# Performance work log

Hardware: AMD Instinct MI355X
Metric: run time of the kernel (lower is better)

The kernel has to match this reference:

```python
import jax, jax.numpy as jnp
import numpy as np

N_HEAD = 16
WINDOW = 256


def setup_inputs() -> dict:
    key = jax.random.key(0)
    ks = jax.random.split(key, 3)
    B, S, D = 2, 2048, 1024
    x = jax.random.normal(ks[0], (B, S, D), dtype=jnp.float32)
    w_attn = jax.random.normal(ks[1], (D, 3 * D), dtype=jnp.float32) * 0.02
    b_attn = jnp.zeros((3 * D,), dtype=jnp.float32)
    w_proj = jax.random.normal(ks[2], (D, D), dtype=jnp.float32) * 0.02
    b_proj = jnp.zeros((D,), dtype=jnp.float32)
    return {"x": x, "w_attn": w_attn, "b_attn": b_attn, "w_proj": w_proj, "b_proj": b_proj}


def reference(x, w_attn, b_attn, w_proj, b_proj):
    B, S, D = x.shape
    hd = D // N_HEAD  # head dim
    scale = 1.0 / np.sqrt(hd).astype(np.float32)

    # fused QKV projection (Conv1D == linear on last dim)
    c = jnp.einsum('bsd,df->bsf', x, w_attn) + b_attn
    q, k, v = jnp.split(c, 3, axis=-1)

    def split_heads(t):  # [B,S,D] -> [B,H,S,hd]
        return t.reshape(B, S, N_HEAD, hd).transpose(0, 2, 1, 3)

    q, k, v = split_heads(q), split_heads(k), split_heads(v)
    present = jnp.stack([k, v], axis=1)  # [B,2,H,S,hd]

    # scores [B,H,S,S]
    w = jnp.einsum('bhqd,bhkd->bhqk', q, k) * scale

    # causal sliding-window mask
    q_pos = jnp.arange(S)[:, None]
    k_pos = jnp.arange(S)[None, :]
    mask = (k_pos <= q_pos) & (k_pos >= q_pos - WINDOW + 1)  # [S,S]
    w = jnp.where(mask[None, None], w, jnp.finfo(w.dtype).min)
    w = jax.nn.softmax(w, axis=-1)

    a = jnp.einsum('bhqk,bhkd->bhqd', w, v)
    a = a.transpose(0, 2, 1, 3).reshape(B, S, D)  # merge heads
    out = jnp.einsum('bsd,df->bsf', a, w_proj) + b_proj
    return out, present
```

## Files before the change

### kernel.cpp

```cpp
#include <hip/hip_runtime.h>
#include <cstdint>
#include <cstddef>

typedef __bf16 bf16x8 __attribute__((ext_vector_type(8)));
typedef float f32x4 __attribute__((ext_vector_type(4)));

#define MFMA16(a, b, c) __builtin_amdgcn_mfma_f32_16x16x32_bf16(a, b, c, 0, 0, 0)

static __device__ __forceinline__ bf16x8 ld_bf16x8(const __bf16* p) {
    return *reinterpret_cast<const bf16x8*>(p);
}

static __device__ __forceinline__ void async_cp16(const __bf16* g, __bf16* l) {
    __builtin_amdgcn_global_load_lds((const __attribute__((address_space(1))) void*)g,
                                     (__attribute__((address_space(3))) void*)l, 16, 0, 0);
}

template <int N>
static __device__ __forceinline__ void wait_vmcnt() {
    asm volatile("s_waitcnt vmcnt(%0)" ::"n"(N) : "memory");
}

static __device__ __forceinline__ void barrier_pinned() {
    __builtin_amdgcn_sched_barrier(0);
    __builtin_amdgcn_s_barrier();
    __builtin_amdgcn_sched_barrier(0);
}

template <int CTRL>
static __device__ __forceinline__ float dppmv(float x) {
    return __builtin_bit_cast(float, __builtin_amdgcn_update_dpp(
        0, __builtin_bit_cast(int, x), CTRL, 0xF, 0xF, true));
}
static __device__ __forceinline__ float rmax16(float x) {
    x = fmaxf(x, dppmv<0x121>(x));
    x = fmaxf(x, dppmv<0x122>(x));
    x = fmaxf(x, dppmv<0x124>(x));
    x = fmaxf(x, dppmv<0x128>(x));
    return x;
}
static __device__ __forceinline__ float rsum16(float x) {
    x += dppmv<0x121>(x);
    x += dppmv<0x122>(x);
    x += dppmv<0x124>(x);
    x += dppmv<0x128>(x);
    return x;
}

__global__ void cvt_kernel(const float* __restrict__ src, __bf16* __restrict__ dst, int n8) {
    int i = blockIdx.x * blockDim.x + threadIdx.x;
    if (i >= n8) return;
    const float4* s4 = reinterpret_cast<const float4*>(src) + (size_t)i * 2;
    float4 a = s4[0], b = s4[1];
    bf16x8 o;
    o[0] = (__bf16)a.x; o[1] = (__bf16)a.y; o[2] = (__bf16)a.z; o[3] = (__bf16)a.w;
    o[4] = (__bf16)b.x; o[5] = (__bf16)b.y; o[6] = (__bf16)b.z; o[7] = (__bf16)b.w;
    reinterpret_cast<bf16x8*>(dst)[i] = o;
}

__global__ __launch_bounds__(256) void tcvt_kernel(const float* __restrict__ in,
                                                   __bf16* __restrict__ out, int K, int N) {
    __shared__ __bf16 T[64][72];
    const int k0 = blockIdx.y * 64, n0 = blockIdx.x * 64;
    const int t = threadIdx.x;
    const int col = (t & 15) << 2;
    const int rowb = t >> 4;
    #pragma unroll
    for (int i = 0; i < 4; i++) {
        int row = i * 16 + rowb;
        float4 v = *reinterpret_cast<const float4*>(&in[(size_t)(k0 + row) * N + n0 + col]);
        T[col + 0][row] = (__bf16)v.x;
        T[col + 1][row] = (__bf16)v.y;
        T[col + 2][row] = (__bf16)v.z;
        T[col + 3][row] = (__bf16)v.w;
    }
    __syncthreads();
    const int oc = (t & 7) << 3;
    const int orb = t >> 3;
    #pragma unroll
    for (int i = 0; i < 2; i++) {
        int r = i * 32 + orb;
        bf16x8 v = *reinterpret_cast<bf16x8*>(&T[r][oc]);
        *reinterpret_cast<bf16x8*>(&out[(size_t)(n0 + r) * K + k0 + oc]) = v;
    }
}

__device__ __forceinline__ void gemm_mainloop(const __bf16* __restrict__ A,
                                              const __bf16* __restrict__ Bt,
                                              int K, int row0, int col0,
                                              __bf16* Als, __bf16* Bls, f32x4 acc[4][4]) {
    const int tid = threadIdx.x;
    const int lane = tid & 63;
    const int wid = tid >> 6;
    const int wr = wid >> 1, wc = wid & 1;
    const int r0 = tid >> 2, o0 = (tid & 3) << 3;
    const __bf16* a0 = A + (size_t)(row0 + r0) * K + o0;
    const __bf16* a1 = A + (size_t)(row0 + r0 + 64) * K + o0;
    const __bf16* b0 = Bt + (size_t)(col0 + r0) * K + o0;
    const __bf16* b1 = Bt + (size_t)(col0 + r0 + 64) * K + o0;
    const int loff = tid * 8;
    const int aoff = (wr * 64 + (lane & 15)) * 32 + ((lane >> 4) << 3);
    const int boff = (wc * 64 + (lane & 15)) * 32 + ((lane >> 4) << 3);

    const int nt = K >> 5;
    async_cp16(a0, &Als[loff]);
    async_cp16(a1, &Als[loff + 2048]);
    async_cp16(b0, &Bls[loff]);
    async_cp16(b1, &Bls[loff + 2048]);
    __syncthreads();

    int cur = 0;
    for (int t = 0; t < nt; ++t) {
        if (t + 1 < nt) {
            const int k1 = (t + 1) << 5;
            const int nb = (cur ^ 1) * 4096;
            async_cp16(a0 + k1, &Als[nb + loff]);
            async_cp16(a1 + k1, &Als[nb + loff + 2048]);
            async_cp16(b0 + k1, &Bls[nb + loff]);
            async_cp16(b1 + k1, &Bls[nb + loff + 2048]);
        }
        const int cb = cur * 4096;
        bf16x8 af[4], bfr[4];
        #pragma unroll
        for (int m = 0; m < 4; m++) af[m] = ld_bf16x8(&Als[cb + aoff + m * 512]);
        #pragma unroll
        for (int n = 0; n < 4; n++) bfr[n] = ld_bf16x8(&Bls[cb + boff + n * 512]);
        #pragma unroll
        for (int m = 0; m < 4; m++) {
            #pragma unroll
            for (int n = 0; n < 4; n++) {
                acc[m][n] = MFMA16(af[m], bfr[n], acc[m][n]);
            }
        }
        __syncthreads();
        cur ^= 1;
    }
}

__global__ __launch_bounds__(256) void gemm_qkv_kernel(const __bf16* __restrict__ xb,
                                                       const __bf16* __restrict__ wabt,
                                                       const float* __restrict__ bias,
                                                       __bf16* __restrict__ qb,
                                                       __bf16* __restrict__ kb,
                                                       __bf16* __restrict__ vt,
                                                       float* __restrict__ present) {
    __shared__ __bf16 Als[2 * 128 * 32];
    __shared__ __bf16 Bls[2 * 128 * 32];
    f32x4 acc[4][4] = {};
    const int row0 = blockIdx.y * 128, col0 = blockIdx.x * 128;
    gemm_mainloop(xb, wabt, 1024, row0, col0, Als, Bls, acc);

    const int lane = threadIdx.x & 63, wid = threadIdx.x >> 6;
    const int wr = wid >> 1, wc = wid & 1;
    const int part = col0 >> 10;
    #pragma unroll
    for (int n = 0; n < 4; n++) {
        int col = col0 + wc * 64 + n * 16 + (lane & 15);
        int hh = (col >> 6) & 15;
        int dd = col & 63;
        float bv = bias[col];
        #pragma unroll
        for (int m = 0; m < 4; m++) {
            #pragma unroll
            for (int r = 0; r < 4; r++) {
                int row = row0 + wr * 64 + m * 16 + ((lane >> 4) << 2) + r;
                int bb = row >> 11, ss = row & 2047;
                float val = acc[m][n][r] + bv;
                size_t qi = (((size_t)(bb * 16 + hh)) * 2048 + ss) * 64 + dd;
                if (part == 0) {
                    qb[qi] = (__bf16)val;
                } else if (part == 1) {
                    kb[qi] = (__bf16)val;
                    present[(((size_t)((bb * 2 + 0) * 16 + hh)) * 2048 + ss) * 64 + dd] = val;
                } else {
                    vt[(((size_t)(bb * 16 + hh)) * 64 + dd) * 2048 + ss] = (__bf16)val;
                    present[(((size_t)((bb * 2 + 1) * 16 + hh)) * 2048 + ss) * 64 + dd] = val;
                }
            }
        }
    }
}

template <int BM, int BN, int WM, int WN>
__device__ __forceinline__ void mainloop2(const __bf16* __restrict__ A,
                                          const __bf16* __restrict__ Bt,
                                          int K, int row0, int col0,
                                          __bf16* lds,
                                          f32x4 (&acc)[BM / WM / 16][BN / WN / 16]) {
    constexpr int MR = BM / WM / 16, NR = BN / WN / 16;
    constexpr int AE = BM * 32;
    constexpr int BUFE = AE + BN * 32;
    constexpr int AI = BM / 16;
    constexpr int BI = BN / 16;
    constexpr int APW = AI / 8;
    constexpr int BPW = BI / 8;
    const int tid = threadIdx.x, l = tid & 63, w = tid >> 6;
    const int wm = w / WN, wn = w % WN;
    const int lr = l >> 2, lc = (l & 3) << 3;
    const int fr = l & 15, fc = (l >> 4) << 3;

    const size_t arow = (size_t)(row0 + lr) * K + lc;
    const size_t brow = (size_t)(col0 + lr) * K + lc;
    const int nt = K >> 5;

    auto stage = [&](int t, int buf) {
        const int k0 = t << 5;
        const int bb = buf * BUFE;
        #pragma unroll
        for (int j = 0; j < APW; j++) {
            const int mi = w * APW + j;
            async_cp16(A + arow + (size_t)mi * 16 * K + k0, lds + bb + mi * 512 + l * 8);
        }
        #pragma unroll
        for (int j = 0; j < BPW; j++) {
            const int ni = w * BPW + j;
            async_cp16(Bt + brow + (size_t)ni * 16 * K + k0, lds + bb + AE + ni * 512 + l * 8);
        }
    };

    stage(0, 0);
    stage(1, 1);

    const int aoff = (wm * (BM / WM) + fr) * 32 + fc;
    const int boff = AE + (wn * (BN / WN) + fr) * 32 + fc;

    int p = 0;
    for (int t = 0; t < nt; ++t) {
        if (t + 1 < nt) {
            wait_vmcnt<APW + BPW>();
        } else {
            wait_vmcnt<0>();
        }
        barrier_pinned();
        if (t + 2 < nt) {
            int p2 = p + 2; if (p2 >= 3) p2 -= 3;
            stage(t + 2, p2);
        }
        const int cb = p * BUFE;
        bf16x8 af[MR], bfv[NR];
        #pragma unroll
        for (int m = 0; m < MR; m++) af[m] = ld_bf16x8(&lds[cb + aoff + m * 512]);
        #pragma unroll
        for (int n = 0; n < NR; n++) bfv[n] = ld_bf16x8(&lds[cb + boff + n * 512]);
        __builtin_amdgcn_s_setprio(1);
        #pragma unroll
        for (int m = 0; m < MR; m++) {
            #pragma unroll
            for (int n = 0; n < NR; n++) {
                acc[m][n] = MFMA16(af[m], bfv[n], acc[m][n]);
            }
        }
        __builtin_amdgcn_s_setprio(0);
        asm volatile("s_waitcnt lgkmcnt(0)" ::: "memory");
        __builtin_amdgcn_sched_barrier(0);
        p = (p == 2) ? 0 : p + 1;
    }
}

__global__ __launch_bounds__(512, 2) void gemm_proj_kernel(const __bf16* __restrict__ ab,
                                                           const __bf16* __restrict__ wpbt,
                                                           const float* __restrict__ bias,
                                                           float* __restrict__ out) {
    __shared__ __bf16 lds[3 * (128 * 32 + 128 * 32)];
    f32x4 acc[2][4] = {};
    const int row0 = blockIdx.y * 128, col0 = blockIdx.x * 128;
    mainloop2<128, 128, 4, 2>(ab, wpbt, 1024, row0, col0, lds, acc);

    const int lane = threadIdx.x & 63, w = threadIdx.x >> 6;
    const int wm = w >> 1, wn = w & 1;
    #pragma unroll
    for (int n = 0; n < 4; n++) {
        int col = col0 + wn * 64 + n * 16 + (lane & 15);
        float bv = bias[col];
        #pragma unroll
        for (int m = 0; m < 2; m++) {
            #pragma unroll
            for (int r = 0; r < 4; r++) {
                int row = row0 + wm * 32 + m * 16 + ((lane >> 4) << 2) + r;
                out[(size_t)row * 1024 + col] = acc[m][n][r] + bv;
            }
        }
    }
}

__global__ __launch_bounds__(256) void attn_kernel(const __bf16* __restrict__ qb,
                                                   const __bf16* __restrict__ kb,
                                                   const __bf16* __restrict__ vtb,
                                                   __bf16* __restrict__ ab) {
    __shared__ __bf16 Pls[4][16 * 40];
    const int bh = blockIdx.x >> 5;
    const int qt = blockIdx.x & 31;
    const int lane = threadIdx.x & 63, wid = threadIdx.x >> 6;
    const int q0w = qt * 64 + wid * 16;

    const __bf16* Qh = qb + (size_t)bh * 2048 * 64;
    const __bf16* Kh = kb + (size_t)bh * 2048 * 64;
    const __bf16* Vt = vtb + (size_t)bh * 64 * 2048;
    __bf16* Pw = &Pls[wid][0];

    bf16x8 qf[2];
    {
        int qr = q0w + (lane & 15);
        const __bf16* qp = Qh + (size_t)qr * 64 + ((lane >> 4) << 3);
        qf[0] = ld_bf16x8(qp);
        qf[1] = ld_bf16x8(qp + 32);
    }

    f32x4 o[4];
    #pragma unroll
    for (int dt = 0; dt < 4; dt++) o[dt] = (f32x4){0.f, 0.f, 0.f, 0.f};
    float mrun[4] = {-1e30f, -1e30f, -1e30f, -1e30f};
    float srun[4] = {0.f, 0.f, 0.f, 0.f};

    const float cl2 = 0.18033688f;
    int klo = q0w - 255;
    int kt0 = klo > 0 ? (klo & ~31) : 0;

    for (int kt = kt0; kt <= q0w + 15; kt += 32) {
        f32x4 s[2];
        #pragma unroll
        for (int kc = 0; kc < 2; kc++) {
            int krow = kt + kc * 16 + (lane & 15);
            const __bf16* kp = Kh + (size_t)krow * 64 + ((lane >> 4) << 3);
            bf16x8 kf0 = ld_bf16x8(kp);
            bf16x8 kf1 = ld_bf16x8(kp + 32);
            f32x4 a = (f32x4){0.f, 0.f, 0.f, 0.f};
            a = MFMA16(qf[0], kf0, a);
            a = MFMA16(qf[1], kf1, a);
            s[kc] = a;
        }
        const bool clean = (kt >= q0w - 240) && (kt + 31 <= q0w);
        float p0v[4], p1v[4], factor[4];
        if (clean) {
            #pragma unroll
            for (int r = 0; r < 4; r++) {
                float s0 = s[0][r] * cl2;
                float s1 = s[1][r] * cl2;
                float mx = rmax16(fmaxf(s0, s1));
                float mn = fmaxf(mrun[r], mx);
                float f = exp2f(mrun[r] - mn);
                float p0 = exp2f(s0 - mn);
                float p1 = exp2f(s1 - mn);
                float ps = rsum16(p0 + p1);
                srun[r] = srun[r] * f + ps;
                mrun[r] = mn;
                factor[r] = f;
                p0v[r] = p0;
                p1v[r] = p1;
            }
        } else {
            #pragma unroll
            for (int r = 0; r < 4; r++) {
                int q = q0w + ((lane >> 4) << 2) + r;
                int k0i = kt + (lane & 15);
                int k1i = k0i + 16;
                bool ok0 = (k0i <= q) && (k0i > q - 256);
                bool ok1 = (k1i <= q) && (k1i > q - 256);
                float s0 = ok0 ? s[0][r] * cl2 : -1e30f;
                float s1 = ok1 ? s[1][r] * cl2 : -1e30f;
                float mx = rmax16(fmaxf(s0, s1));
                float mn = fmaxf(mrun[r], mx);
                float f = exp2f(mrun[r] - mn);
                float p0 = ok0 ? exp2f(s0 - mn) : 0.f;
                float p1 = ok1 ? exp2f(s1 - mn) : 0.f;
                float ps = rsum16(p0 + p1);
                srun[r] = srun[r] * f + ps;
                mrun[r] = mn;
                factor[r] = f;
                p0v[r] = p0;
                p1v[r] = p1;
            }
        }
        #pragma unroll
        for (int dt = 0; dt < 4; dt++) {
            #pragma unroll
            for (int r = 0; r < 4; r++) o[dt][r] *= factor[r];
        }
        #pragma unroll
        for (int r = 0; r < 4; r++) {
            int qrow = ((lane >> 4) << 2) + r;
            Pw[qrow * 40 + (lane & 15)] = (__bf16)p0v[r];
            Pw[qrow * 40 + 16 + (lane & 15)] = (__bf16)p1v[r];
        }
        asm volatile("s_waitcnt lgkmcnt(0)" ::: "memory");
        bf16x8 pf = ld_bf16x8(&Pw[(lane & 15) * 40 + ((lane >> 4) << 3)]);
        #pragma unroll
        for (int dt = 0; dt < 4; dt++) {
            bf16x8 vf = ld_bf16x8(&Vt[(size_t)(dt * 16 + (lane & 15)) * 2048 + kt + ((lane >> 4) << 3)]);
            o[dt] = MFMA16(pf, vf, o[dt]);
        }
    }

    const int bb = bh >> 4, hh = bh & 15;
    #pragma unroll
    for (int r = 0; r < 4; r++) {
        int q = q0w + ((lane >> 4) << 2) + r;
        float inv = 1.f / srun[r];
        size_t base = ((size_t)bb * 2048 + q) * 1024 + hh * 64;
        #pragma unroll
        for (int dt = 0; dt < 4; dt++) {
            ab[base + dt * 16 + (lane & 15)] = (__bf16)(o[dt][r] * inv);
        }
    }
}

extern "C" void kernel_launch(void* const* d_in, const int* in_sizes, int n_in,
                              void* d_out, int out_size, void* d_ws, size_t ws_size,
                              hipStream_t stream) {
    const float* x = (const float*)d_in[0];
    const float* w_attn = (const float*)d_in[1];
    const float* b_attn = (const float*)d_in[2];
    const float* w_proj = (const float*)d_in[3];
    const float* b_proj = (const float*)d_in[4];

    float* out = (float*)d_out;
    float* present = out + (size_t)2 * 2048 * 1024;

    char* w = (char*)d_ws;
    __bf16* xb   = (__bf16*)(w);
    __bf16* wabt = (__bf16*)(w + 8388608);
    __bf16* wpbt = (__bf16*)(w + 14680064);
    __bf16* qb   = (__bf16*)(w + 16777216);
    __bf16* kb   = (__bf16*)(w + 25165824);
    __bf16* vt   = (__bf16*)(w + 33554432);
    __bf16* ab   = xb;

    cvt_kernel<<<2048, 256, 0, stream>>>(x, xb, 524288);
    tcvt_kernel<<<dim3(48, 16), 256, 0, stream>>>(w_attn, wabt, 1024, 3072);
    tcvt_kernel<<<dim3(16, 16), 256, 0, stream>>>(w_proj, wpbt, 1024, 1024);

    gemm_qkv_kernel<<<dim3(24, 32), 256, 0, stream>>>(xb, wabt, b_attn, qb, kb, vt, present);

    attn_kernel<<<1024, 256, 0, stream>>>(qb, kb, vt, ab);

    gemm_proj_kernel<<<dim3(8, 32), 512, 0, stream>>>(ab, wpbt, b_proj, out);
}
```

Before: 121.7 us.

## Port QKV GEMM to swizzled triple-buffered mainloop; add lazy softmax rescale and V prefetch

The QKV projection GEMM now uses the templated triple-buffered mainloop with 512 threads (8 waves), vmcnt-based waits and an XOR swizzle of LDS columns to avoid bank conflicts. The proj GEMM shares this mainloop, so it also gets the swizzle. In attention, V fragments are loaded at the start of each key tile so the global latency overlaps the QK^T and softmax work. For clean tiles, the running max and the rescale of the output accumulator are skipped when every lane's new max grows by at most 8 (log2 domain). That cuts exp and multiply work but lets values exceed the running max by up to 2^8 before renormalising, which is a precision risk.

After: 123.0 us. Within noise of the previous version (+1.0%).

```diff
diff --git a/kernel.cpp b/kernel.cpp
--- a/kernel.cpp
+++ b/kernel.cpp
@@ -85,85 +85,108 @@
     }
 }
 
-__device__ __forceinline__ void gemm_mainloop(const __bf16* __restrict__ A,
-                                              const __bf16* __restrict__ Bt,
-                                              int K, int row0, int col0,
-                                              __bf16* Als, __bf16* Bls, f32x4 acc[4][4]) {
-    const int tid = threadIdx.x;
-    const int lane = tid & 63;
-    const int wid = tid >> 6;
-    const int wr = wid >> 1, wc = wid & 1;
-    const int r0 = tid >> 2, o0 = (tid & 3) << 3;
-    const __bf16* a0 = A + (size_t)(row0 + r0) * K + o0;
-    const __bf16* a1 = A + (size_t)(row0 + r0 + 64) * K + o0;
-    const __bf16* b0 = Bt + (size_t)(col0 + r0) * K + o0;
-    const __bf16* b1 = Bt + (size_t)(col0 + r0 + 64) * K + o0;
-    const int loff = tid * 8;
-    const int aoff = (wr * 64 + (lane & 15)) * 32 + ((lane >> 4) << 3);
-    const int boff = (wc * 64 + (lane & 15)) * 32 + ((lane >> 4) << 3);
-
+template <int BM, int BN, int WM, int WN>
+__device__ __forceinline__ void mainloop2(const __bf16* __restrict__ A,
+                                          const __bf16* __restrict__ Bt,
+                                          int K, int row0, int col0,
+                                          __bf16* lds,
+                                          f32x4 (&acc)[BM / WM / 16][BN / WN / 16]) {
+    constexpr int MR = BM / WM / 16, NR = BN / WN / 16;
+    constexpr int AE = BM * 32;
+    constexpr int BUFE = AE + BN * 32;
+    constexpr int APW = BM / 16 / 8;
+    constexpr int BPW = BN / 16 / 8;
+    const int tid = threadIdx.x, l = tid & 63, w = tid >> 6;
+    const int wm = w / WN, wn = w % WN;
+    const int lr = l >> 2;
+    const int lcs = (((l & 3) ^ ((l >> 3) & 3)) << 3);
+    const int fr = l & 15;
+    const int fc = (((l >> 4) ^ ((l >> 1) & 3)) << 3);
+
+    const size_t arow = (size_t)(row0 + lr) * K + lcs;
+    const size_t brow = (size_t)(col0 + lr) * K + lcs;
     const int nt = K >> 5;
-    async_cp16(a0, &Als[loff]);
-    async_cp16(a1, &Als[loff + 2048]);
-    async_cp16(b0, &Bls[loff]);
-    async_cp16(b1, &Bls[loff + 2048]);
-    __syncthreads();
-
-    int cur = 0;
+
+    auto stage = [&](int t, int buf) {
+        const int k0 = t << 5;
+        const int bb = buf * BUFE;
+        #pragma unroll
+        for (int j = 0; j < APW; j++) {
+            const int mi = w * APW + j;
+            async_cp16(A + arow + (size_t)mi * 16 * K + k0, lds + bb + mi * 512 + l * 8);
+        }
+        #pragma unroll
+        for (int j = 0; j < BPW; j++) {
+            const int ni = w * BPW + j;
+            async_cp16(Bt + brow + (size_t)ni * 16 * K + k0, lds + bb + AE + ni * 512 + l * 8);
+        }
+    };
+
+    stage(0, 0);
+    stage(1, 1);
+
+    const int aoff = (wm * (BM / WM) + fr) * 32 + fc;
+    const int boff = AE + (wn * (BN / WN) + fr) * 32 + fc;
+
+    int p = 0;
     for (int t = 0; t < nt; ++t) {
         if (t + 1 < nt) {
-            const int k1 = (t + 1) << 5;
-            const int nb = (cur ^ 1) * 4096;
-            async_cp16(a0 + k1, &Als[nb + loff]);
-            async_cp16(a1 + k1, &Als[nb + loff + 2048]);
-            async_cp16(b0 + k1, &Bls[nb + loff]);
-            async_cp16(b1 + k1, &Bls[nb + loff + 2048]);
-        }
-        const int cb = cur * 4096;
-        bf16x8 af[4], bfr[4];
-        #pragma unroll
-        for (int m = 0; m < 4; m++) af[m] = ld_bf16x8(&Als[cb + aoff + m * 512]);
-        #pragma unroll
-        for (int n = 0; n < 4; n++) bfr[n] = ld_bf16x8(&Bls[cb + boff + n * 512]);
-        #pragma unroll
-        for (int m = 0; m < 4; m++) {
-            #pragma unroll
-            for (int n = 0; n < 4; n++) {
-                acc[m][n] = MFMA16(af[m], bfr[n], acc[m][n]);
-            }
-        }
-        __syncthreads();
-        cur ^= 1;
-    }
-}
-
-__global__ __launch_bounds__(256) void gemm_qkv_kernel(const __bf16* __restrict__ xb,
-                                                       const __bf16* __restrict__ wabt,
-                                                       const float* __restrict__ bias,
-                                                       __bf16* __restrict__ qb,
-                                                       __bf16* __restrict__ kb,
-                                                       __bf16* __restrict__ vt,
-                                                       float* __restrict__ present) {
-    __shared__ __bf16 Als[2 * 128 * 32];
-    __shared__ __bf16 Bls[2 * 128 * 32];
-    f32x4 acc[4][4] = {};
+            wait_vmcnt<APW + BPW>();
+        } else {
+            wait_vmcnt<0>();
+        }
+        barrier_pinned();
+        if (t + 2 < nt) {
+            int p2 = p + 2; if (p2 >= 3) p2 -= 3;
+            stage(t + 2, p2);
+        }
+        const int cb = p * BUFE;
+        bf16x8 af[MR], bfv[NR];
+        #pragma unroll
+        for (int m = 0; m < MR; m++) af[m] = ld_bf16x8(&lds[cb + aoff + m * 512]);
+        #pragma unroll
+        for (int n = 0; n < NR; n++) bfv[n] = ld_bf16x8(&lds[cb + boff + n * 512]);
+        __builtin_amdgcn_s_setprio(1);
+        #pragma unroll
+        for (int m = 0; m < MR; m++) {
+            #pragma unroll
+            for (int n = 0; n < NR; n++) {
+                acc[m][n] = MFMA16(af[m], bfv[n], acc[m][n]);
+            }
+        }
+        __builtin_amdgcn_s_setprio(0);
+        asm volatile("s_waitcnt lgkmcnt(0)" ::: "memory");
+        __builtin_amdgcn_sched_barrier(0);
+        p = (p == 2) ? 0 : p + 1;
+    }
+}
+
+__global__ __launch_bounds__(512, 2) void gemm_qkv_kernel(const __bf16* __restrict__ xb,
+                                                          const __bf16* __restrict__ wabt,
+                                                          const float* __restrict__ bias,
+                                                          __bf16* __restrict__ qb,
+                                                          __bf16* __restrict__ kb,
+                                                          __bf16* __restrict__ vt,
+                                                          float* __restrict__ present) {
+    __shared__ __bf16 lds[3 * (128 * 32 + 128 * 32)];
+    f32x4 acc[2][4] = {};
     const int row0 = blockIdx.y * 128, col0 = blockIdx.x * 128;
-    gemm_mainloop(xb, wabt, 1024, row0, col0, Als, Bls, acc);
-
-    const int lane = threadIdx.x & 63, wid = threadIdx.x >> 6;
-    const int wr = wid >> 1, wc = wid & 1;
+    mainloop2<128, 128, 4, 2>(xb, wabt, 1024, row0, col0, lds, acc);
+
+    const int l = threadIdx.x & 63, w = threadIdx.x >> 6;
+    const int wm = w >> 1, wn = w & 1;
     const int part = col0 >> 10;
     #pragma unroll
     for (int n = 0; n < 4; n++) {
-        int col = col0 + wc * 64 + n * 16 + (lane & 15);
+        int col = col0 + wn * 64 + n * 16 + (l & 15);
         int hh = (col >> 6) & 15;
         int dd = col & 63;
         float bv = bias[col];
         #pragma unroll
-        for (int m = 0; m < 4; m++) {
+        for (int m = 0; m < 2; m++) {
             #pragma unroll
             for (int r = 0; r < 4; r++) {
-                int row = row0 + wr * 64 + m * 16 + ((lane >> 4) << 2) + r;
+                int row = row0 + wm * 32 + m * 16 + ((l >> 4) << 2) + r;
                 int bb = row >> 11, ss = row & 2047;
                 float val = acc[m][n][r] + bv;
                 size_t qi = (((size_t)(bb * 16 + hh)) * 2048 + ss) * 64 + dd;
@@ -181,82 +204,6 @@
     }
 }
 
-template <int BM, int BN, int WM, int WN>
-__device__ __forceinline__ void mainloop2(const __bf16* __restrict__ A,
-                                          const __bf16* __restrict__ Bt,
-                                          int K, int row0, int col0,
-                                          __bf16* lds,
-                                          f32x4 (&acc)[BM / WM / 16][BN / WN / 16]) {
-    constexpr int MR = BM / WM / 16, NR = BN / WN / 16;
-    constexpr int AE = BM * 32;
-    constexpr int BUFE = AE + BN * 32;
-    constexpr int AI = BM / 16;
-    constexpr int BI = BN / 16;
-    constexpr int APW = AI / 8;
-    constexpr int BPW = BI / 8;
-    const int tid = threadIdx.x, l = tid & 63, w = tid >> 6;
-    const int wm = w / WN, wn = w % WN;
-    const int lr = l >> 2, lc = (l & 3) << 3;
-    const int fr = l & 15, fc = (l >> 4) << 3;
-
-    const size_t arow = (size_t)(row0 + lr) * K + lc;
-    const size_t brow = (size_t)(col0 + lr) * K + lc;
-    const int nt = K >> 5;
-
-    auto stage = [&](int t, int buf) {
-        const int k0 = t << 5;
-        const int bb = buf * BUFE;
-        #pragma unroll
-        for (int j = 0; j < APW; j++) {
-            const int mi = w * APW + j;
-            async_cp16(A + arow + (size_t)mi * 16 * K + k0, lds + bb + mi * 512 + l * 8);
-        }
-        #pragma unroll
-        for (int j = 0; j < BPW; j++) {
-            const int ni = w * BPW + j;
-            async_cp16(Bt + brow + (size_t)ni * 16 * K + k0, lds + bb + AE + ni * 512 + l * 8);
-        }
-    };
-
-    stage(0, 0);
-    stage(1, 1);
-
-    const int aoff = (wm * (BM / WM) + fr) * 32 + fc;
-    const int boff = AE + (wn * (BN / WN) + fr) * 32 + fc;
-
-    int p = 0;
-    for (int t = 0; t < nt; ++t) {
-        if (t + 1 < nt) {
-            wait_vmcnt<APW + BPW>();
-        } else {
-            wait_vmcnt<0>();
-        }
-        barrier_pinned();
-        if (t + 2 < nt) {
-            int p2 = p + 2; if (p2 >= 3) p2 -= 3;
-            stage(t + 2, p2);
-        }
-        const int cb = p * BUFE;
-        bf16x8 af[MR], bfv[NR];
-        #pragma unroll
-        for (int m = 0; m < MR; m++) af[m] = ld_bf16x8(&lds[cb + aoff + m * 512]);
-        #pragma unroll
-        for (int n = 0; n < NR; n++) bfv[n] = ld_bf16x8(&lds[cb + boff + n * 512]);
-        __builtin_amdgcn_s_setprio(1);
-        #pragma unroll
-        for (int m = 0; m < MR; m++) {
-            #pragma unroll
-            for (int n = 0; n < NR; n++) {
-                acc[m][n] = MFMA16(af[m], bfv[n], acc[m][n]);
-            }
-        }
-        __builtin_amdgcn_s_setprio(0);
-        asm volatile("s_waitcnt lgkmcnt(0)" ::: "memory");
-        __builtin_amdgcn_sched_barrier(0);
-        p = (p == 2) ? 0 : p + 1;
-    }
-}
-
 __global__ __launch_bounds__(512, 2) void gemm_proj_kernel(const __bf16* __restrict__ ab,
                                                            const __bf16* __restrict__ wpbt,
                                                            const float* __restrict__ bias,
@@ -317,6 +264,10 @@
     int kt0 = klo > 0 ? (klo & ~31) : 0;
 
     for (int kt = kt0; kt <= q0w + 15; kt += 32) {
+        bf16x8 vf[4];
+        #pragma unroll
+        for (int dt = 0; dt < 4; dt++)
+            vf[dt] = ld_bf16x8(&Vt[(size_t)(dt * 16 + (lane & 15)) * 2048 + kt + ((lane >> 4) << 3)]);
         f32x4 s[2];
         #pragma unroll
         for (int kc = 0; kc < 2; kc++) {
@@ -330,25 +281,48 @@
             s[kc] = a;
         }
         const bool clean = (kt >= q0w - 240) && (kt + 31 <= q0w);
-        float p0v[4], p1v[4], factor[4];
+        float p0v[4], p1v[4];
         if (clean) {
+            float s0v[4], s1v[4], mx[4];
             #pragma unroll
             for (int r = 0; r < 4; r++) {
-                float s0 = s[0][r] * cl2;
-                float s1 = s[1][r] * cl2;
-                float mx = rmax16(fmaxf(s0, s1));
-                float mn = fmaxf(mrun[r], mx);
-                float f = exp2f(mrun[r] - mn);
-                float p0 = exp2f(s0 - mn);
-                float p1 = exp2f(s1 - mn);
-                float ps = rsum16(p0 + p1);
-                srun[r] = srun[r] * f + ps;
-                mrun[r] = mn;
-                factor[r] = f;
-                p0v[r] = p0;
-                p1v[r] = p1;
+                s0v[r] = s[0][r] * cl2;
+                s1v[r] = s[1][r] * cl2;
+                mx[r] = rmax16(fmaxf(s0v[r], s1v[r]));
+            }
+            float grow = fmaxf(fmaxf(mx[0] - mrun[0], mx[1] - mrun[1]),
+                               fmaxf(mx[2] - mrun[2], mx[3] - mrun[3]));
+            if (__all(grow <= 8.f)) {
+                #pragma unroll
+                for (int r = 0; r < 4; r++) {
+                    float p0 = exp2f(s0v[r] - mrun[r]);
+                    float p1 = exp2f(s1v[r] - mrun[r]);
+                    srun[r] += rsum16(p0 + p1);
+                    p0v[r] = p0;
+                    p1v[r] = p1;
+                }
+            } else {
+                float factor[4];
+                #pragma unroll
+                for (int r = 0; r < 4; r++) {
+                    float mn = fmaxf(mrun[r], mx[r]);
+                    float f = exp2f(mrun[r] - mn);
+                    float p0 = exp2f(s0v[r] - mn);
+                    float p1 = exp2f(s1v[r] - mn);
+                    srun[r] = srun[r] * f + rsum16(p0 + p1);
+                    mrun[r] = mn;
+                    factor[r] = f;
+                    p0v[r] = p0;
+                    p1v[r] = p1;
+                }
+                #pragma unroll
+                for (int dt = 0; dt < 4; dt++) {
+                    #pragma unroll
+                    for (int r = 0; r < 4; r++) o[dt][r] *= factor[r];
+                }
             }
         } else {
+            float factor[4];
             #pragma unroll
             for (int r = 0; r < 4; r++) {
                 int q = q0w + ((lane >> 4) << 2) + r;
@@ -363,18 +337,17 @@
                 float f = exp2f(mrun[r] - mn);
                 float p0 = ok0 ? exp2f(s0 - mn) : 0.f;
                 float p1 = ok1 ? exp2f(s1 - mn) : 0.f;
-                float ps = rsum16(p0 + p1);
-                srun[r] = srun[r] * f + ps;
+                srun[r] = srun[r] * f + rsum16(p0 + p1);
                 mrun[r] = mn;
                 factor[r] = f;
                 p0v[r] = p0;
                 p1v[r] = p1;
             }
-        }
-        #pragma unroll
-        for (int dt = 0; dt < 4; dt++) {
-            #pragma unroll
-            for (int r = 0; r < 4; r++) o[dt][r] *= factor[r];
+            #pragma unroll
+            for (int dt = 0; dt < 4; dt++) {
+                #pragma unroll
+                for (int r = 0; r < 4; r++) o[dt][r] *= factor[r];
+            }
         }
         #pragma unroll
         for (int r = 0; r < 4; r++) {
@@ -386,8 +359,7 @@
         bf16x8 pf = ld_bf16x8(&Pw[(lane & 15) * 40 + ((lane >> 4) << 3)]);
         #pragma unroll
         for (int dt = 0; dt < 4; dt++) {
-            bf16x8 vf = ld_bf16x8(&Vt[(size_t)(dt * 16 + (lane & 15)) * 2048 + kt + ((lane >> 4) << 3)]);
-            o[dt] = MFMA16(pf, vf, o[dt]);
+            o[dt] = MFMA16(pf, vf[dt], o[dt]);
         }
     }
 
@@ -429,7 +401,7 @@
     tcvt_kernel<<<dim3(48, 16), 256, 0, stream>>>(w_attn, wabt, 1024, 3072);
     tcvt_kernel<<<dim3(16, 16), 256, 0, stream>>>(w_proj, wpbt, 1024, 1024);
 
-    gemm_qkv_kernel<<<dim3(24, 32), 256, 0, stream>>>(xb, wabt, b_attn, qb, kb, vt, present);
+    gemm_qkv_kernel<<<dim3(24, 32), 512, 0, stream>>>(xb, wabt, b_attn, qb, kb, vt, present);
 
     attn_kernel<<<1024, 256, 0, stream>>>(qb, kb, vt, ab);
 
```
